# Optimization experiments

Hardware: AMD Instinct MI355X
Metric: run time of the kernel (lower is better)

The kernel has to match this reference:

```python
import jax, jax.numpy as jnp
import numpy as np
import math

B, NQ, NK = 32, 1024, 1024
DQ = DK = DV = 512
H = 8
EPS = 1e-5


def _layernorm(x, g, b):
    mu = jnp.mean(x, axis=-1, keepdims=True)
    var = jnp.mean(jnp.square(x - mu), axis=-1, keepdims=True)
    return (x - mu) * jax.lax.rsqrt(var + EPS) * g + b


def setup_inputs() -> dict:
    key = jax.random.key(0)
    ks = jax.random.split(key, 8)
    s = 0.03  # small init scale for linear weights
    return {
        "Q": jax.random.normal(ks[0], (B, NQ, DQ), jnp.float32),
        "K": jax.random.normal(ks[1], (B, NK, DK), jnp.float32),
        "Wq": jax.random.normal(ks[2], (DQ, DV), jnp.float32) * s,
        "bq": jnp.zeros((DV,), jnp.float32),
        "Wk": jax.random.normal(ks[3], (DK, DV), jnp.float32) * s,
        "bk": jnp.zeros((DV,), jnp.float32),
        "Wv": jax.random.normal(ks[4], (DK, DV), jnp.float32) * s,
        "bv": jnp.zeros((DV,), jnp.float32),
        "Wo": jax.random.normal(ks[5], (DV, DV), jnp.float32) * s,
        "bo": jnp.zeros((DV,), jnp.float32),
        "g0": jnp.ones((DV,), jnp.float32),
        "beta0": jnp.zeros((DV,), jnp.float32),
        "g1": jnp.ones((DV,), jnp.float32),
        "beta1": jnp.zeros((DV,), jnp.float32),
    }


def reference(Q, K, Wq, bq, Wk, bk, Wv, bv, Wo, bo, g0, beta0, g1, beta1):
    b, nq, _ = Q.shape
    nk = K.shape[1]
    d = DV // H  # head dim (dim_split)

    q = Q @ Wq + bq            # [B, Nq, DV]
    k = K @ Wk + bk            # [B, Nk, DV]
    v = K @ Wv + bv            # [B, Nk, DV]

    # torch.cat(x.split(d, 2), 0) == reshape to [B,N,H,d] then stack heads on batch dim
    qh = q.reshape(b, nq, H, d).transpose(2, 0, 1, 3)  # [H, B, Nq, d]
    kh = k.reshape(b, nk, H, d).transpose(2, 0, 1, 3)  # [H, B, Nk, d]
    vh = v.reshape(b, nk, H, d).transpose(2, 0, 1, 3)  # [H, B, Nk, d]

    # NOTE: scaled by sqrt(dim_V), and softmax over the QUERY axis (torch dim=1)
    scores = jnp.einsum('hbqd,hbkd->hbqk', qh, kh) / math.sqrt(DV)
    A = jax.nn.softmax(scores, axis=2)                 # over Nq (faithful to source)
    oh = qh + jnp.einsum('hbqk,hbkd->hbqd', A, vh)     # residual on Q_

    out = oh.transpose(1, 2, 0, 3).reshape(b, nq, DV)  # merge heads back
    out = _layernorm(out, g0, beta0)
    out = out + jax.nn.relu(out @ Wo + bo)
    out = _layernorm(out, g1, beta1)
    return out
```

## Files before the change

kernel.cpp:

```cpp
#include <hip/hip_runtime.h>

#define Bz  32
#define NQz 1024
#define NKz 1024
#define SCALE 0.04419417382415922f

typedef __bf16 bf16_t;
typedef bf16_t bf16x8 __attribute__((ext_vector_type(8)));
typedef bf16_t bf16x4 __attribute__((ext_vector_type(4)));
typedef float  f32x4  __attribute__((ext_vector_type(4)));

#define MFMA16(a, b, c) __builtin_amdgcn_mfma_f32_16x16x32_bf16(a, b, c, 0, 0, 0)

__device__ __forceinline__ void gll16(const void* g, void* l) {
  __builtin_amdgcn_global_load_lds(
      (const __attribute__((address_space(1))) void*)g,
      (__attribute__((address_space(3))) void*)l, 16, 0, 0);
}

__device__ __forceinline__ bf16x8 cvt8(float4 a, float4 b) {
  bf16x8 r;
  r[0] = (bf16_t)a.x; r[1] = (bf16_t)a.y; r[2] = (bf16_t)a.z; r[3] = (bf16_t)a.w;
  r[4] = (bf16_t)b.x; r[5] = (bf16_t)b.y; r[6] = (bf16_t)b.z; r[7] = (bf16_t)b.w;
  return r;
}

__global__ void transpose_w(const float* __restrict__ W0, const float* __restrict__ W1,
                            const float* __restrict__ W2, const float* __restrict__ W3,
                            bf16_t* __restrict__ out) {
  __shared__ float tile[32][33];
  const float* W = blockIdx.z == 0 ? W0 : blockIdx.z == 1 ? W1 : blockIdx.z == 2 ? W2 : W3;
  bf16_t* o = out + (size_t)blockIdx.z * 512 * 512;
  const int n0 = blockIdx.x * 32, k0 = blockIdx.y * 32;
  const int tx = threadIdx.x, ty = threadIdx.y;
  for (int i = 0; i < 4; i++)
    tile[ty + i * 8][tx] = W[(size_t)(k0 + ty + i * 8) * 512 + n0 + tx];
  __syncthreads();
  for (int i = 0; i < 4; i++)
    o[(size_t)(n0 + ty + i * 8) * 512 + k0 + tx] = (bf16_t)tile[tx][ty + i * 8];
}

template <int DUAL>
__global__ __launch_bounds__(256) void gemm_f32a(const float* __restrict__ A,
                                                 const bf16_t* __restrict__ Wt,
                                                 const float* __restrict__ b0v,
                                                 const float* __restrict__ b1v,
                                                 float mult0,
                                                 bf16_t* __restrict__ C0,
                                                 bf16_t* __restrict__ C1) {
  __shared__ __align__(16) bf16_t As[128][40];
  __shared__ __align__(16) bf16_t Bs[128 * 32];
  const int t = threadIdx.x;
  const int wave = t >> 6, lane = t & 63;
  const int quad = lane >> 4, l16 = lane & 15;
  const int wm = wave & 1, wn = wave >> 1;
  const int m0 = blockIdx.x * 128, n0 = blockIdx.y * 128;
  const int r = t >> 1, half = t & 1;
  const int drow = lane >> 2;
  const int dg = (lane & 3) ^ ((lane >> 3) & 3);

  f32x4 acc[4][4] = {};

  for (int k0 = 0; k0 < 512; k0 += 32) {
    __syncthreads();
    for (int p = 0; p < 2; p++) {
      const bf16_t* src = Wt + (size_t)(n0 + p * 64 + wave * 16 + drow) * 512 + k0 + dg * 8;
      gll16(src, &Bs[(p * 256 + wave * 64) * 8]);
    }
    {
      const float* ap = A + (size_t)(m0 + r) * 512 + k0 + half * 16;
      float4 a0 = *(const float4*)(ap + 0);
      float4 a1 = *(const float4*)(ap + 4);
      float4 a2 = *(const float4*)(ap + 8);
      float4 a3 = *(const float4*)(ap + 12);
      *(bf16x8*)&As[r][half * 16 + 0] = cvt8(a0, a1);
      *(bf16x8*)&As[r][half * 16 + 8] = cvt8(a2, a3);
    }
    __syncthreads();
    bf16x8 af[4], bfv[4];
    for (int mt = 0; mt < 4; mt++)
      af[mt] = *(const bf16x8*)&As[wm * 64 + mt * 16 + l16][quad * 8];
    for (int nt = 0; nt < 4; nt++) {
      const int rB = wn * 64 + nt * 16 + l16;
      bfv[nt] = *(const bf16x8*)&Bs[rB * 32 + ((quad ^ ((rB >> 1) & 3)) * 8)];
    }
    for (int mt = 0; mt < 4; mt++)
      for (int nt = 0; nt < 4; nt++)
        acc[mt][nt] = MFMA16(af[mt], bfv[nt], acc[mt][nt]);
  }

  const float* bias = (!DUAL || n0 < 512) ? b0v : b1v;
  bf16_t* C = (!DUAL || n0 < 512) ? C0 : C1;
  const float mult = (!DUAL || n0 < 512) ? mult0 : 1.0f;
  const int nb = (!DUAL || n0 < 512) ? n0 : n0 - 512;
  for (int mt = 0; mt < 4; mt++) {
    for (int nt = 0; nt < 4; nt++) {
      const int row = m0 + wm * 64 + mt * 16 + quad * 4;
      const int col = nb + wn * 64 + nt * 16 + l16;
      const float bv = bias[col];
      for (int rg = 0; rg < 4; rg++)
        C[(size_t)(row + rg) * 512 + col] = (bf16_t)((acc[mt][nt][rg] + bv) * mult);
    }
  }
}

__global__ __launch_bounds__(256) void gemm_bf16a(const bf16_t* __restrict__ A,
                                                  const bf16_t* __restrict__ Wt,
                                                  const float* __restrict__ bias,
                                                  bf16_t* __restrict__ C) {
  __shared__ __align__(16) bf16_t As[128][40];
  __shared__ __align__(16) bf16_t Bs[128 * 32];
  const int t = threadIdx.x;
  const int wave = t >> 6, lane = t & 63;
  const int quad = lane >> 4, l16 = lane & 15;
  const int wm = wave & 1, wn = wave >> 1;
  const int m0 = blockIdx.x * 128, n0 = blockIdx.y * 128;
  const int r = t >> 1, half = t & 1;
  const int drow = lane >> 2;
  const int dg = (lane & 3) ^ ((lane >> 3) & 3);

  f32x4 acc[4][4] = {};

  for (int k0 = 0; k0 < 512; k0 += 32) {
    __syncthreads();
    for (int p = 0; p < 2; p++) {
      const bf16_t* src = Wt + (size_t)(n0 + p * 64 + wave * 16 + drow) * 512 + k0 + dg * 8;
      gll16(src, &Bs[(p * 256 + wave * 64) * 8]);
    }
    {
      const bf16_t* ap = A + (size_t)(m0 + r) * 512 + k0 + half * 16;
      *(bf16x8*)&As[r][half * 16 + 0] = *(const bf16x8*)(ap + 0);
      *(bf16x8*)&As[r][half * 16 + 8] = *(const bf16x8*)(ap + 8);
    }
    __syncthreads();
    bf16x8 af[4], bfv[4];
    for (int mt = 0; mt < 4; mt++)
      af[mt] = *(const bf16x8*)&As[wm * 64 + mt * 16 + l16][quad * 8];
    for (int nt = 0; nt < 4; nt++) {
      const int rB = wn * 64 + nt * 16 + l16;
      bfv[nt] = *(const bf16x8*)&Bs[rB * 32 + ((quad ^ ((rB >> 1) & 3)) * 8)];
    }
    for (int mt = 0; mt < 4; mt++)
      for (int nt = 0; nt < 4; nt++)
        acc[mt][nt] = MFMA16(af[mt], bfv[nt], acc[mt][nt]);
  }

  for (int mt = 0; mt < 4; mt++) {
    for (int nt = 0; nt < 4; nt++) {
      const int row = m0 + wm * 64 + mt * 16 + quad * 4;
      const int col = n0 + wn * 64 + nt * 16 + l16;
      const float bv = bias[col];
      for (int rg = 0; rg < 4; rg++) {
        float v = acc[mt][nt][rg] + bv;
        float x = (float)A[(size_t)(row + rg) * 512 + col];
        C[(size_t)(row + rg) * 512 + col] = (bf16_t)(x + fmaxf(v, 0.f));
      }
    }
  }
}

__global__ __launch_bounds__(256) void attn_stats(const bf16_t* __restrict__ qp,
                                                  const bf16_t* __restrict__ kp,
                                                  const bf16_t* __restrict__ vp,
                                                  bf16_t* __restrict__ Vt) {
  __shared__ __align__(16) bf16_t Vs[128][72];
  __shared__ __align__(16) bf16_t Qs[64 * 64];
  __shared__ float ls[128];
  const int t = threadIdx.x;
  const int wave = t >> 6, lane = t & 63;
  const int quad = lane >> 4, l16 = lane & 15;
  const int id = blockIdx.x;
  const int kb = ((id >> 3) & 7) * 128;
  const int hb = (id & 7) * 32 + (id >> 6);
  const int h = hb >> 5, b = hb & 31;
  const bf16_t* qbase = qp + (size_t)b * NQz * 512 + h * 64;
  const bf16_t* kbase = kp + (size_t)b * NKz * 512 + h * 64;
  const int drow = lane >> 3;
  const int dg = (lane & 7) ^ drow;

  {
    const int r = t >> 1, half = t & 1;
    const bf16_t* vr = vp + (size_t)b * NKz * 512 + (size_t)(kb + r) * 512 + h * 64 + half * 32;
    *(bf16x8*)&Vs[r][half * 32 + 0]  = *(const bf16x8*)(vr + 0);
    *(bf16x8*)&Vs[r][half * 32 + 8]  = *(const bf16x8*)(vr + 8);
    *(bf16x8*)&Vs[r][half * 32 + 16] = *(const bf16x8*)(vr + 16);
    *(bf16x8*)&Vs[r][half * 32 + 24] = *(const bf16x8*)(vr + 24);
  }

  bf16x8 aK[2][2];
  for (int mt = 0; mt < 2; mt++) {
    const bf16_t* kr = kbase + (size_t)(kb + wave * 32 + mt * 16 + l16) * 512 + quad * 8;
    aK[mt][0] = *(const bf16x8*)kr;
    aK[mt][1] = *(const bf16x8*)(kr + 32);
  }

  f32x4 lacc[2] = {};
  for (int q0 = 0; q0 < NQz; q0 += 64) {
    __syncthreads();
    for (int p = 0; p < 2; p++) {
      const bf16_t* src = qbase + (size_t)(q0 + p * 32 + wave * 8 + drow) * 512 + dg * 8;
      gll16(src, &Qs[(p * 256 + wave * 64) * 8]);
    }
    __syncthreads();
    for (int nt = 0; nt < 4; nt++) {
      const int rQ = nt * 16 + l16;
      bf16x8 b0 = *(const bf16x8*)&Qs[rQ * 64 + ((quad ^ (rQ & 7)) * 8)];
      bf16x8 b1 = *(const bf16x8*)&Qs[rQ * 64 + (((quad + 4) ^ (rQ & 7)) * 8)];
      for (int mt = 0; mt < 2; mt++) {
        f32x4 s = {0.f, 0.f, 0.f, 0.f};
        s = MFMA16(aK[mt][0], b0, s);
        s = MFMA16(aK[mt][1], b1, s);
        lacc[mt][0] += __expf(s[0]);
        lacc[mt][1] += __expf(s[1]);
        lacc[mt][2] += __expf(s[2]);
        lacc[mt][3] += __expf(s[3]);
      }
    }
  }
  for (int mt = 0; mt < 2; mt++) {
    for (int rg = 0; rg < 4; rg++) {
      float v = lacc[mt][rg];
      v += __shfl_xor(v, 1);
      v += __shfl_xor(v, 2);
      v += __shfl_xor(v, 4);
      v += __shfl_xor(v, 8);
      if (l16 == 0) ls[wave * 32 + mt * 16 + quad * 4 + rg] = 1.0f / v;
    }
  }
  __syncthreads();
  const int d = t >> 2, kc = (t & 3) * 32;
  bf16_t* vtr = Vt + (size_t)hb * 64 * 1024 + (size_t)d * 1024 + kb + kc;
  for (int c = 0; c < 4; c++) {
    bf16x8 o;
    for (int j = 0; j < 8; j++)
      o[j] = (bf16_t)((float)Vs[kc + c * 8 + j][d] * ls[kc + c * 8 + j]);
    *(bf16x8*)(vtr + c * 8) = o;
  }
}

__global__ __launch_bounds__(256) void attn_out(const bf16_t* __restrict__ qp,
                                                const bf16_t* __restrict__ kp,
                                                const bf16_t* __restrict__ Vt,
                                                bf16_t* __restrict__ oh) {
  __shared__ __align__(16) bf16_t Ks[64 * 64];
  __shared__ __align__(16) bf16_t Vts[64 * 64];
  __shared__ __align__(16) bf16_t Ps[128][72];
  const int t = threadIdx.x;
  const int wave = t >> 6, lane = t & 63;
  const int quad = lane >> 4, l16 = lane & 15;
  const int id = blockIdx.x;
  const int qt = (id >> 3) & 7;
  const int hb = (id & 7) * 32 + (id >> 6);
  const int h = hb >> 5, b = hb & 31;
  const int q0 = qt * 128;
  const bf16_t* qbase = qp + (size_t)b * NQz * 512 + h * 64;
  const bf16_t* kbase = kp + (size_t)b * NKz * 512 + h * 64;
  const bf16_t* vtbase = Vt + (size_t)hb * 64 * 1024;
  const int drow = lane >> 3;
  const int dg = (lane & 7) ^ drow;

  bf16x8 bQ[2][2];
  for (int nt = 0; nt < 2; nt++) {
    const bf16_t* qr = qbase + (size_t)(q0 + wave * 32 + nt * 16 + l16) * 512 + quad * 8;
    bQ[nt][0] = *(const bf16x8*)qr;
    bQ[nt][1] = *(const bf16x8*)(qr + 32);
  }

  f32x4 acc[2][4] = {};
  for (int kk = 0; kk < NKz; kk += 64) {
    __syncthreads();
    for (int p = 0; p < 2; p++) {
      const bf16_t* ksrc = kbase + (size_t)(kk + p * 32 + wave * 8 + drow) * 512 + dg * 8;
      gll16(ksrc, &Ks[(p * 256 + wave * 64) * 8]);
      const bf16_t* vsrc = vtbase + (size_t)(p * 32 + wave * 8 + drow) * 1024 + kk + dg * 8;
      gll16(vsrc, &Vts[(p * 256 + wave * 64) * 8]);
    }
    __syncthreads();
    for (int mt = 0; mt < 4; mt++) {
      const int rK = mt * 16 + l16;
      bf16x8 a0 = *(const bf16x8*)&Ks[rK * 64 + ((quad ^ (rK & 7)) * 8)];
      bf16x8 a1 = *(const bf16x8*)&Ks[rK * 64 + (((quad + 4) ^ (rK & 7)) * 8)];
      for (int nt = 0; nt < 2; nt++) {
        f32x4 s = {0.f, 0.f, 0.f, 0.f};
        s = MFMA16(a0, bQ[nt][0], s);
        s = MFMA16(a1, bQ[nt][1], s);
        bf16x4 pk;
        pk[0] = (bf16_t)__expf(s[0]);
        pk[1] = (bf16_t)__expf(s[1]);
        pk[2] = (bf16_t)__expf(s[2]);
        pk[3] = (bf16_t)__expf(s[3]);
        *(bf16x4*)&Ps[wave * 32 + nt * 16 + l16][mt * 16 + quad * 4] = pk;
      }
    }
    bf16x8 aP[2][2];
    for (int mt = 0; mt < 2; mt++) {
      aP[mt][0] = *(const bf16x8*)&Ps[wave * 32 + mt * 16 + l16][quad * 8];
      aP[mt][1] = *(const bf16x8*)&Ps[wave * 32 + mt * 16 + l16][quad * 8 + 32];
    }
    for (int nd = 0; nd < 4; nd++) {
      const int rV = nd * 16 + l16;
      bf16x8 b0 = *(const bf16x8*)&Vts[rV * 64 + ((quad ^ (rV & 7)) * 8)];
      bf16x8 b1 = *(const bf16x8*)&Vts[rV * 64 + (((quad + 4) ^ (rV & 7)) * 8)];
      for (int mt = 0; mt < 2; mt++) {
        acc[mt][nd] = MFMA16(aP[mt][0], b0, acc[mt][nd]);
        acc[mt][nd] = MFMA16(aP[mt][1], b1, acc[mt][nd]);
      }
    }
  }
  for (int mt = 0; mt < 2; mt++)
    for (int nd = 0; nd < 4; nd++)
      for (int rg = 0; rg < 4; rg++)
        Ps[wave * 32 + mt * 16 + quad * 4 + rg][nd * 16 + l16] = (bf16_t)acc[mt][nd][rg];
  const int row = wave * 32 + (lane >> 1), cc = (lane & 1) * 32;
  bf16_t* orow = oh + ((size_t)b * NQz + q0 + row) * 512 + h * 64 + cc;
  for (int c = 0; c < 4; c++)
    *(bf16x8*)(orow + c * 8) = *(const bf16x8*)&Ps[row][cc + c * 8];
}

template <int RES, int F32OUT>
__global__ __launch_bounds__(256) void ln_k(const bf16_t* __restrict__ x,
                                            const bf16_t* __restrict__ res,
                                            const float* __restrict__ g,
                                            const float* __restrict__ be,
                                            bf16_t* __restrict__ yb,
                                            float* __restrict__ yf) {
  const int wave = threadIdx.x >> 6, lane = threadIdx.x & 63;
  const size_t row = (size_t)blockIdx.x * 4 + wave;
  bf16x8 xv = *(const bf16x8*)(x + row * 512 + lane * 8);
  float xf[8];
  for (int i = 0; i < 8; i++) xf[i] = (float)xv[i];
  if (RES) {
    bf16x8 rv = *(const bf16x8*)(res + row * 512 + lane * 8);
    for (int i = 0; i < 8; i++) xf[i] += (float)rv[i];
  }
  float s = 0.f, sq = 0.f;
  for (int i = 0; i < 8; i++) { s += xf[i]; sq += xf[i] * xf[i]; }
  for (int off = 1; off < 64; off <<= 1) {
    s += __shfl_xor(s, off);
    sq += __shfl_xor(sq, off);
  }
  const float mu = s * (1.0f / 512.0f);
  const float var = sq * (1.0f / 512.0f) - mu * mu;
  const float rstd = rsqrtf(var + 1e-5f);
  float4 gv0 = *(const float4*)(g + lane * 8);
  float4 gv1 = *(const float4*)(g + lane * 8 + 4);
  float4 bv0 = *(const float4*)(be + lane * 8);
  float4 bv1 = *(const float4*)(be + lane * 8 + 4);
  float gg[8] = {gv0.x, gv0.y, gv0.z, gv0.w, gv1.x, gv1.y, gv1.z, gv1.w};
  float bb[8] = {bv0.x, bv0.y, bv0.z, bv0.w, bv1.x, bv1.y, bv1.z, bv1.w};
  float o[8];
  for (int i = 0; i < 8; i++) o[i] = (xf[i] - mu) * rstd * gg[i] + bb[i];
  if (F32OUT) {
    float4 o0 = {o[0], o[1], o[2], o[3]}, o1 = {o[4], o[5], o[6], o[7]};
    *(float4*)(yf + row * 512 + lane * 8) = o0;
    *(float4*)(yf + row * 512 + lane * 8 + 4) = o1;
  } else {
    bf16x8 ov;
    for (int i = 0; i < 8; i++) ov[i] = (bf16_t)o[i];
    *(bf16x8*)(yb + row * 512 + lane * 8) = ov;
  }
}

extern "C" void kernel_launch(void* const* d_in, const int* in_sizes, int n_in,
                              void* d_out, int out_size, void* d_ws, size_t ws_size,
                              hipStream_t stream) {
  (void)in_sizes; (void)n_in; (void)out_size; (void)ws_size;
  const float* Q   = (const float*)d_in[0];
  const float* K   = (const float*)d_in[1];
  const float* Wq  = (const float*)d_in[2];
  const float* bq  = (const float*)d_in[3];
  const float* Wk  = (const float*)d_in[4];
  const float* bk  = (const float*)d_in[5];
  const float* Wv  = (const float*)d_in[6];
  const float* bv  = (const float*)d_in[7];
  const float* Wo  = (const float*)d_in[8];
  const float* bo  = (const float*)d_in[9];
  const float* g0  = (const float*)d_in[10];
  const float* be0 = (const float*)d_in[11];
  const float* g1  = (const float*)d_in[12];
  const float* be1 = (const float*)d_in[13];
  float* outp = (float*)d_out;

  char* w = (char*)d_ws;
  bf16_t* Wt  = (bf16_t*)w;
  bf16_t* qp  = (bf16_t*)(w + (2ull << 20));
  bf16_t* kp  = (bf16_t*)(w + (34ull << 20));
  bf16_t* vp  = (bf16_t*)(w + (66ull << 20));
  bf16_t* Vt  = (bf16_t*)(w + (98ull << 20));
  bf16_t* ohb = (bf16_t*)(w + (130ull << 20));
  bf16_t* x0b = vp;
  bf16_t* oh2 = kp;

  transpose_w<<<dim3(16, 16, 4), dim3(32, 8), 0, stream>>>(Wq, Wk, Wv, Wo, Wt);
  gemm_f32a<0><<<dim3(256, 4), 256, 0, stream>>>(Q, Wt, bq, nullptr, 1.0f, qp, nullptr);
  gemm_f32a<1><<<dim3(256, 8), 256, 0, stream>>>(K, Wt + (1 << 18), bk, bv, SCALE, kp, vp);
  attn_stats<<<2048, 256, 0, stream>>>(qp, kp, vp, Vt);
  attn_out<<<2048, 256, 0, stream>>>(qp, kp, Vt, ohb);
  ln_k<1, 0><<<8192, 256, 0, stream>>>(ohb, qp, g0, be0, x0b, nullptr);
  gemm_bf16a<<<dim3(256, 4), 256, 0, stream>>>(x0b, Wt + 3 * (1 << 18), bo, oh2);
  ln_k<0, 1><<<8192, 256, 0, stream>>>(oh2, nullptr, g1, be1, nullptr, outp);
}
```

Baseline: 493.9 us.

## Double-buffer LDS tiles in GEMM and attention kernels; fold log2e into exp2

Converts the GEMM, attention-stats and attention-output loops to double-buffered LDS tiles. The next tile's global loads are issued before the current tile is computed, and explicit vmcnt waits plus raw s_barrier replace the paired __syncthreads. Separately, the key projection scale now includes log2(e) so the softmax exponentials can use the hardware exp2 instruction directly instead of __expf. This doubles LDS per block, which may lower occupancy, and relies on hand-counted vmcnt values being correct.

```diff
diff --git a/kernel.cpp b/kernel.cpp
--- a/kernel.cpp
+++ b/kernel.cpp
@@ -12,10 +12,24 @@
 
 #define MFMA16(a, b, c) __builtin_amdgcn_mfma_f32_16x16x32_bf16(a, b, c, 0, 0, 0)
 
+#define SBAR() asm volatile("s_barrier" ::: "memory")
+#define WAITVM(n) asm volatile("s_waitcnt vmcnt(" #n ")" ::: "memory")
+#define WAITVL(n) asm volatile("s_waitcnt vmcnt(" #n ") lgkmcnt(0)" ::: "memory")
+
 __device__ __forceinline__ void gll16(const void* g, void* l) {
   __builtin_amdgcn_global_load_lds(
       (const __attribute__((address_space(1))) void*)g,
       (__attribute__((address_space(3))) void*)l, 16, 0, 0);
+}
+
+__device__ __forceinline__ float fexp2(float x) {
+#if __has_builtin(__builtin_amdgcn_exp2f)
+  return __builtin_amdgcn_exp2f(x);
+#else
+  float r;
+  asm("v_exp_f32 %0, %1" : "=v"(r) : "v"(x));
+  return r;
+#endif
 }
 
 __device__ __forceinline__ bf16x8 cvt8(float4 a, float4 b) {
@@ -49,7 +63,7 @@
                                                  bf16_t* __restrict__ C0,
                                                  bf16_t* __restrict__ C1) {
   __shared__ __align__(16) bf16_t As[128][40];
-  __shared__ __align__(16) bf16_t Bs[128 * 32];
+  __shared__ __align__(16) bf16_t Bs[2][128 * 32];
   const int t = threadIdx.x;
   const int wave = t >> 6, lane = t & 63;
   const int quad = lane >> 4, l16 = lane & 15;
@@ -61,32 +75,46 @@
 
   f32x4 acc[4][4] = {};
 
-  for (int k0 = 0; k0 < 512; k0 += 32) {
-    __syncthreads();
-    for (int p = 0; p < 2; p++) {
-      const bf16_t* src = Wt + (size_t)(n0 + p * 64 + wave * 16 + drow) * 512 + k0 + dg * 8;
-      gll16(src, &Bs[(p * 256 + wave * 64) * 8]);
-    }
-    {
-      const float* ap = A + (size_t)(m0 + r) * 512 + k0 + half * 16;
-      float4 a0 = *(const float4*)(ap + 0);
-      float4 a1 = *(const float4*)(ap + 4);
-      float4 a2 = *(const float4*)(ap + 8);
-      float4 a3 = *(const float4*)(ap + 12);
-      *(bf16x8*)&As[r][half * 16 + 0] = cvt8(a0, a1);
-      *(bf16x8*)&As[r][half * 16 + 8] = cvt8(a2, a3);
-    }
-    __syncthreads();
+  const float* arow = A + (size_t)(m0 + r) * 512 + half * 16;
+  const bf16_t* wrow = Wt + (size_t)(n0 + wave * 16 + drow) * 512 + dg * 8;
+
+  for (int p = 0; p < 2; p++)
+    gll16(wrow + (size_t)(p * 64) * 512, &Bs[0][(p * 256 + wave * 64) * 8]);
+  float4 a0 = *(const float4*)(arow + 0);
+  float4 a1 = *(const float4*)(arow + 4);
+  float4 a2 = *(const float4*)(arow + 8);
+  float4 a3 = *(const float4*)(arow + 12);
+
+  for (int it = 0; it < 16; it++) {
+    const int cur = it & 1;
+    if (it < 15)
+      for (int p = 0; p < 2; p++)
+        gll16(wrow + (it + 1) * 32 + (size_t)(p * 64) * 512,
+              &Bs[cur ^ 1][(p * 256 + wave * 64) * 8]);
+    *(bf16x8*)&As[r][half * 16 + 0] = cvt8(a0, a1);
+    *(bf16x8*)&As[r][half * 16 + 8] = cvt8(a2, a3);
+    if (it < 15) {
+      const float* ap = arow + (it + 1) * 32;
+      a0 = *(const float4*)(ap + 0);
+      a1 = *(const float4*)(ap + 4);
+      a2 = *(const float4*)(ap + 8);
+      a3 = *(const float4*)(ap + 12);
+      WAITVL(6);
+    } else {
+      WAITVL(0);
+    }
+    SBAR();
     bf16x8 af[4], bfv[4];
     for (int mt = 0; mt < 4; mt++)
       af[mt] = *(const bf16x8*)&As[wm * 64 + mt * 16 + l16][quad * 8];
     for (int nt = 0; nt < 4; nt++) {
       const int rB = wn * 64 + nt * 16 + l16;
-      bfv[nt] = *(const bf16x8*)&Bs[rB * 32 + ((quad ^ ((rB >> 1) & 3)) * 8)];
+      bfv[nt] = *(const bf16x8*)&Bs[cur][rB * 32 + ((quad ^ ((rB >> 1) & 3)) * 8)];
     }
     for (int mt = 0; mt < 4; mt++)
       for (int nt = 0; nt < 4; nt++)
         acc[mt][nt] = MFMA16(af[mt], bfv[nt], acc[mt][nt]);
+    SBAR();
   }
 
   const float* bias = (!DUAL || n0 < 512) ? b0v : b1v;
@@ -109,7 +137,7 @@
                                                   const float* __restrict__ bias,
                                                   bf16_t* __restrict__ C) {
   __shared__ __align__(16) bf16_t As[128][40];
-  __shared__ __align__(16) bf16_t Bs[128 * 32];
+  __shared__ __align__(16) bf16_t Bs[2][128 * 32];
   const int t = threadIdx.x;
   const int wave = t >> 6, lane = t & 63;
   const int quad = lane >> 4, l16 = lane & 15;
@@ -121,28 +149,42 @@
 
   f32x4 acc[4][4] = {};
 
-  for (int k0 = 0; k0 < 512; k0 += 32) {
-    __syncthreads();
-    for (int p = 0; p < 2; p++) {
-      const bf16_t* src = Wt + (size_t)(n0 + p * 64 + wave * 16 + drow) * 512 + k0 + dg * 8;
-      gll16(src, &Bs[(p * 256 + wave * 64) * 8]);
-    }
-    {
-      const bf16_t* ap = A + (size_t)(m0 + r) * 512 + k0 + half * 16;
-      *(bf16x8*)&As[r][half * 16 + 0] = *(const bf16x8*)(ap + 0);
-      *(bf16x8*)&As[r][half * 16 + 8] = *(const bf16x8*)(ap + 8);
-    }
-    __syncthreads();
+  const bf16_t* arow = A + (size_t)(m0 + r) * 512 + half * 16;
+  const bf16_t* wrow = Wt + (size_t)(n0 + wave * 16 + drow) * 512 + dg * 8;
+
+  for (int p = 0; p < 2; p++)
+    gll16(wrow + (size_t)(p * 64) * 512, &Bs[0][(p * 256 + wave * 64) * 8]);
+  bf16x8 v0 = *(const bf16x8*)(arow + 0);
+  bf16x8 v1 = *(const bf16x8*)(arow + 8);
+
+  for (int it = 0; it < 16; it++) {
+    const int cur = it & 1;
+    if (it < 15)
+      for (int p = 0; p < 2; p++)
+        gll16(wrow + (it + 1) * 32 + (size_t)(p * 64) * 512,
+              &Bs[cur ^ 1][(p * 256 + wave * 64) * 8]);
+    *(bf16x8*)&As[r][half * 16 + 0] = v0;
+    *(bf16x8*)&As[r][half * 16 + 8] = v1;
+    if (it < 15) {
+      const bf16_t* ap = arow + (it + 1) * 32;
+      v0 = *(const bf16x8*)(ap + 0);
+      v1 = *(const bf16x8*)(ap + 8);
+      WAITVL(4);
+    } else {
+      WAITVL(0);
+    }
+    SBAR();
     bf16x8 af[4], bfv[4];
     for (int mt = 0; mt < 4; mt++)
       af[mt] = *(const bf16x8*)&As[wm * 64 + mt * 16 + l16][quad * 8];
     for (int nt = 0; nt < 4; nt++) {
       const int rB = wn * 64 + nt * 16 + l16;
-      bfv[nt] = *(const bf16x8*)&Bs[rB * 32 + ((quad ^ ((rB >> 1) & 3)) * 8)];
+      bfv[nt] = *(const bf16x8*)&Bs[cur][rB * 32 + ((quad ^ ((rB >> 1) & 3)) * 8)];
     }
     for (int mt = 0; mt < 4; mt++)
       for (int nt = 0; nt < 4; nt++)
         acc[mt][nt] = MFMA16(af[mt], bfv[nt], acc[mt][nt]);
+    SBAR();
   }
 
   for (int mt = 0; mt < 4; mt++) {
@@ -164,7 +206,7 @@
                                                   const bf16_t* __restrict__ vp,
                                                   bf16_t* __restrict__ Vt) {
   __shared__ __align__(16) bf16_t Vs[128][72];
-  __shared__ __align__(16) bf16_t Qs[64 * 64];
+  __shared__ __align__(16) bf16_t Qs[2][64 * 64];
   __shared__ float ls[128];
   const int t = threadIdx.x;
   const int wave = t >> 6, lane = t & 63;
@@ -194,28 +236,40 @@
     aK[mt][1] = *(const bf16x8*)(kr + 32);
   }
 
+  for (int p = 0; p < 2; p++) {
+    const bf16_t* src = qbase + (size_t)(p * 32 + wave * 8 + drow) * 512 + dg * 8;
+    gll16(src, &Qs[0][(p * 256 + wave * 64) * 8]);
+  }
+
   f32x4 lacc[2] = {};
-  for (int q0 = 0; q0 < NQz; q0 += 64) {
-    __syncthreads();
-    for (int p = 0; p < 2; p++) {
-      const bf16_t* src = qbase + (size_t)(q0 + p * 32 + wave * 8 + drow) * 512 + dg * 8;
-      gll16(src, &Qs[(p * 256 + wave * 64) * 8]);
-    }
-    __syncthreads();
+  for (int it = 0; it < 16; it++) {
+    const int cur = it & 1;
+    if (it < 15) {
+      const int qn = (it + 1) * 64;
+      for (int p = 0; p < 2; p++) {
+        const bf16_t* src = qbase + (size_t)(qn + p * 32 + wave * 8 + drow) * 512 + dg * 8;
+        gll16(src, &Qs[cur ^ 1][(p * 256 + wave * 64) * 8]);
+      }
+      WAITVM(2);
+    } else {
+      WAITVM(0);
+    }
+    SBAR();
     for (int nt = 0; nt < 4; nt++) {
       const int rQ = nt * 16 + l16;
-      bf16x8 b0 = *(const bf16x8*)&Qs[rQ * 64 + ((quad ^ (rQ & 7)) * 8)];
-      bf16x8 b1 = *(const bf16x8*)&Qs[rQ * 64 + (((quad + 4) ^ (rQ & 7)) * 8)];
+      bf16x8 b0 = *(const bf16x8*)&Qs[cur][rQ * 64 + ((quad ^ (rQ & 7)) * 8)];
+      bf16x8 b1 = *(const bf16x8*)&Qs[cur][rQ * 64 + (((quad + 4) ^ (rQ & 7)) * 8)];
       for (int mt = 0; mt < 2; mt++) {
         f32x4 s = {0.f, 0.f, 0.f, 0.f};
         s = MFMA16(aK[mt][0], b0, s);
         s = MFMA16(aK[mt][1], b1, s);
-        lacc[mt][0] += __expf(s[0]);
-        lacc[mt][1] += __expf(s[1]);
-        lacc[mt][2] += __expf(s[2]);
-        lacc[mt][3] += __expf(s[3]);
-      }
-    }
+        lacc[mt][0] += fexp2(s[0]);
+        lacc[mt][1] += fexp2(s[1]);
+        lacc[mt][2] += fexp2(s[2]);
+        lacc[mt][3] += fexp2(s[3]);
+      }
+    }
+    SBAR();
   }
   for (int mt = 0; mt < 2; mt++) {
     for (int rg = 0; rg < 4; rg++) {
@@ -242,8 +296,8 @@
                                                 const bf16_t* __restrict__ kp,
                                                 const bf16_t* __restrict__ Vt,
                                                 bf16_t* __restrict__ oh) {
-  __shared__ __align__(16) bf16_t Ks[64 * 64];
-  __shared__ __align__(16) bf16_t Vts[64 * 64];
+  __shared__ __align__(16) bf16_t Ks[2][64 * 64];
+  __shared__ __align__(16) bf16_t Vts[2][64 * 64];
   __shared__ __align__(16) bf16_t Ps[128][72];
   const int t = threadIdx.x;
   const int wave = t >> 6, lane = t & 63;
@@ -266,29 +320,43 @@
     bQ[nt][1] = *(const bf16x8*)(qr + 32);
   }
 
+  for (int p = 0; p < 2; p++) {
+    const bf16_t* ksrc = kbase + (size_t)(p * 32 + wave * 8 + drow) * 512 + dg * 8;
+    gll16(ksrc, &Ks[0][(p * 256 + wave * 64) * 8]);
+    const bf16_t* vsrc = vtbase + (size_t)(p * 32 + wave * 8 + drow) * 1024 + dg * 8;
+    gll16(vsrc, &Vts[0][(p * 256 + wave * 64) * 8]);
+  }
+
   f32x4 acc[2][4] = {};
-  for (int kk = 0; kk < NKz; kk += 64) {
-    __syncthreads();
-    for (int p = 0; p < 2; p++) {
-      const bf16_t* ksrc = kbase + (size_t)(kk + p * 32 + wave * 8 + drow) * 512 + dg * 8;
-      gll16(ksrc, &Ks[(p * 256 + wave * 64) * 8]);
-      const bf16_t* vsrc = vtbase + (size_t)(p * 32 + wave * 8 + drow) * 1024 + kk + dg * 8;
-      gll16(vsrc, &Vts[(p * 256 + wave * 64) * 8]);
-    }
-    __syncthreads();
+  for (int it = 0; it < 16; it++) {
+    const int kk = it * 64;
+    const int cur = it & 1;
+    if (it < 15) {
+      const int kn = kk + 64;
+      for (int p = 0; p < 2; p++) {
+        const bf16_t* ksrc = kbase + (size_t)(kn + p * 32 + wave * 8 + drow) * 512 + dg * 8;
+        gll16(ksrc, &Ks[cur ^ 1][(p * 256 + wave * 64) * 8]);
+        const bf16_t* vsrc = vtbase + (size_t)(p * 32 + wave * 8 + drow) * 1024 + kn + dg * 8;
+        gll16(vsrc, &Vts[cur ^ 1][(p * 256 + wave * 64) * 8]);
+      }
+      WAITVM(4);
+    } else {
+      WAITVM(0);
+    }
+    SBAR();
     for (int mt = 0; mt < 4; mt++) {
       const int rK = mt * 16 + l16;
-      bf16x8 a0 = *(const bf16x8*)&Ks[rK * 64 + ((quad ^ (rK & 7)) * 8)];
-      bf16x8 a1 = *(const bf16x8*)&Ks[rK * 64 + (((quad + 4) ^ (rK & 7)) * 8)];
+      bf16x8 a0 = *(const bf16x8*)&Ks[cur][rK * 64 + ((quad ^ (rK & 7)) * 8)];
+      bf16x8 a1 = *(const bf16x8*)&Ks[cur][rK * 64 + (((quad + 4) ^ (rK & 7)) * 8)];
       for (int nt = 0; nt < 2; nt++) {
         f32x4 s = {0.f, 0.f, 0.f, 0.f};
         s = MFMA16(a0, bQ[nt][0], s);
         s = MFMA16(a1, bQ[nt][1], s);
         bf16x4 pk;
-        pk[0] = (bf16_t)__expf(s[0]);
-        pk[1] = (bf16_t)__expf(s[1]);
-        pk[2] = (bf16_t)__expf(s[2]);
-        pk[3] = (bf16_t)__expf(s[3]);
+        pk[0] = (bf16_t)fexp2(s[0]);
+        pk[1] = (bf16_t)fexp2(s[1]);
+        pk[2] = (bf16_t)fexp2(s[2]);
+        pk[3] = (bf16_t)fexp2(s[3]);
         *(bf16x4*)&Ps[wave * 32 + nt * 16 + l16][mt * 16 + quad * 4] = pk;
       }
     }
@@ -299,13 +367,14 @@
     }
     for (int nd = 0; nd < 4; nd++) {
       const int rV = nd * 16 + l16;
-      bf16x8 b0 = *(const bf16x8*)&Vts[rV * 64 + ((quad ^ (rV & 7)) * 8)];
-      bf16x8 b1 = *(const bf16x8*)&Vts[rV * 64 + (((quad + 4) ^ (rV & 7)) * 8)];
+      bf16x8 b0 = *(const bf16x8*)&Vts[cur][rV * 64 + ((quad ^ (rV & 7)) * 8)];
+      bf16x8 b1 = *(const bf16x8*)&Vts[cur][rV * 64 + (((quad + 4) ^ (rV & 7)) * 8)];
       for (int mt = 0; mt < 2; mt++) {
         acc[mt][nd] = MFMA16(aP[mt][0], b0, acc[mt][nd]);
         acc[mt][nd] = MFMA16(aP[mt][1], b1, acc[mt][nd]);
       }
     }
+    SBAR();
   }
   for (int mt = 0; mt < 2; mt++)
     for (int nd = 0; nd < 4; nd++)
@@ -393,7 +462,8 @@
 
   transpose_w<<<dim3(16, 16, 4), dim3(32, 8), 0, stream>>>(Wq, Wk, Wv, Wo, Wt);
   gemm_f32a<0><<<dim3(256, 4), 256, 0, stream>>>(Q, Wt, bq, nullptr, 1.0f, qp, nullptr);
-  gemm_f32a<1><<<dim3(256, 8), 256, 0, stream>>>(K, Wt + (1 << 18), bk, bv, SCALE, kp, vp);
+  gemm_f32a<1><<<dim3(256, 8), 256, 0, stream>>>(K, Wt + (1 << 18), bk, bv,
+                                                 SCALE * 1.4426950408889634f, kp, vp);
   attn_stats<<<2048, 256, 0, stream>>>(qp, kp, vp, Vt);
   attn_out<<<2048, 256, 0, stream>>>(qp, kp, Vt, ohb);
   ln_k<1, 0><<<8192, 256, 0, stream>>>(ohb, qp, g0, be0, x0b, nullptr);
```

New measurement: 492.1 us. No clear change (-0.4%).
